# Kernel optimization log

Measured on AMD Instinct MI355X. Metric: run time of the kernel, lower is better.

The kernel has to match this reference:

```python
import jax, jax.numpy as jnp
import numpy as np

D_MODEL = 1024  # scaling uses sqrt(d_model), as in the source


def setup_inputs() -> dict:
    key = jax.random.key(0)
    kx, kq, kk, kv = jax.random.split(key, 4)
    B, N, D, H = 4, 4096, D_MODEL, 128
    X = jax.random.normal(kx, (B, N, D), dtype=jnp.float32)
    # nn.Linear(d_model, d_head, bias=False) weights, stored as [d_model, d_head]
    s = 1.0 / np.sqrt(D)
    Wq = jax.random.normal(kq, (D, H), dtype=jnp.float32) * s
    Wk = jax.random.normal(kk, (D, H), dtype=jnp.float32) * s
    Wv = jax.random.normal(kv, (D, H), dtype=jnp.float32) * s
    return {"X": X, "Wq": Wq, "Wk": Wk, "Wv": Wv}


def reference(X, Wq, Wk, Wv):
    # Q, K, V: [B, N, H]
    Q = jnp.einsum("bnd,dh->bnh", X, Wq)
    K = jnp.einsum("bnd,dh->bnh", X, Wk)
    V = jnp.einsum("bnd,dh->bnh", X, Wv)
    # Scores: [B, N, N]; source divides by sqrt(d_model) (not sqrt(d_head))
    A = jnp.einsum("bqh,bkh->bqk", Q, K) / jnp.sqrt(jnp.float32(D_MODEL))
    A = jax.nn.softmax(A, axis=-1)
    # Dropout is identity in eval mode (deterministic reference baseline)
    return jnp.einsum("bqk,bkh->bqh", A, V)
```

## Files before the change

### kernel.cpp

```cpp
#include <hip/hip_runtime.h>
#include <stdint.h>

typedef __bf16 bf16_t;
typedef bf16_t bf16x8 __attribute__((ext_vector_type(8)));
typedef float f32x4 __attribute__((ext_vector_type(4)));
typedef float f32x16 __attribute__((ext_vector_type(16)));
typedef unsigned short u16;
typedef unsigned int u32;

#define MFMA16(a, b, c) __builtin_amdgcn_mfma_f32_16x16x32_bf16((a), (b), (c), 0, 0, 0)
#define MFMA32(a, b, c) __builtin_amdgcn_mfma_f32_32x32x16_bf16((a), (b), (c), 0, 0, 0)

#define QSCALE 0.04508422002778633f

__device__ __forceinline__ u16 f2bf(float f) {
  union { float f; unsigned u; } v; v.f = f;
  unsigned r = v.u + 0x7fffu + ((v.u >> 16) & 1u);
  return (u16)(r >> 16);
}

__device__ __forceinline__ float exp2x(float x) {
#if __has_builtin(__builtin_amdgcn_exp2f)
  return __builtin_amdgcn_exp2f(x);
#else
  return exp2f(x);
#endif
}

__device__ __forceinline__ float rcpx(float x) {
#if __has_builtin(__builtin_amdgcn_rcpf)
  return __builtin_amdgcn_rcpf(x);
#else
  return 1.0f / x;
#endif
}

__device__ __forceinline__ void async_cp16(const void* g, void* l) {
  __builtin_amdgcn_global_load_lds(
      (__attribute__((address_space(1))) void*)(void*)g,
      (__attribute__((address_space(3))) void*)l, 16, 0, 0);
}

__device__ __forceinline__ u32 cvtpk(float lo, float hi) {
  u32 r;
  asm("v_cvt_pk_bf16_f32 %0, %1, %2" : "=v"(r) : "v"(lo), "v"(hi));
  return r;
}
__device__ __forceinline__ void pl32swap(u32& a, u32& b) {
  asm volatile("v_permlane32_swap_b32 %0, %1" : "+v"(a), "+v"(b));
}

__global__ __launch_bounds__(256) void pack_w_k(const float* __restrict__ Wq,
                                                const float* __restrict__ Wk,
                                                const float* __restrict__ Wv,
                                                u16* __restrict__ wp) {
  int t = blockIdx.x * 256 + threadIdx.x;
  int mat = t >> 14;
  int rr = t & 16383;
  int frag = rr >> 6, lane = rr & 63;
  int nt = frag >> 5, kc = frag & 31;
  const float* W = (mat == 0) ? Wq : ((mat == 1) ? Wk : Wv);
  int k0 = kc * 32 + ((lane >> 4) << 3);
  int col = nt * 16 + (lane & 15);
  union { u16 h[8]; uint4 q; } u_;
#pragma unroll
  for (int j = 0; j < 8; ++j) u_.h[j] = f2bf(W[(size_t)(k0 + j) * 128 + col]);
  *(uint4*)(wp + (size_t)t * 8) = u_.q;
}

__global__ __launch_bounds__(256) void qkv_k(const float* __restrict__ X,
                                             const u16* __restrict__ wp,
                                             u16* __restrict__ Qb,
                                             u16* __restrict__ Kb,
                                             u16* __restrict__ Vt) {
  __shared__ __align__(16) char xs[2][4096];
  const int tid = threadIdx.x;
  const int w = tid >> 6, lane = tid & 63;
  const int r16 = lane >> 4, c16 = lane & 15;
  const int m0 = blockIdx.x * 32;

  f32x4 acc[2][6];
#pragma unroll
  for (int mt = 0; mt < 2; ++mt)
#pragma unroll
    for (int i = 0; i < 6; ++i) acc[mt][i] = (f32x4){0.f, 0.f, 0.f, 0.f};

  const int srow = tid >> 3, scol = tid & 7;
  const float* sbase = X + (size_t)(m0 + srow) * 1024 + scol * 8;
  const int soff = srow * 128 + ((scol * 16) ^ ((srow & 7) << 4));

  {
    float4 v0 = *(const float4*)(sbase);
    float4 v1 = *(const float4*)(sbase + 4);
    union { u16 h[8]; uint4 q; } u_;
    u_.h[0] = f2bf(v0.x); u_.h[1] = f2bf(v0.y); u_.h[2] = f2bf(v0.z); u_.h[3] = f2bf(v0.w);
    u_.h[4] = f2bf(v1.x); u_.h[5] = f2bf(v1.y); u_.h[6] = f2bf(v1.z); u_.h[7] = f2bf(v1.w);
    *(uint4*)(xs[0] + soff) = u_.q;
  }
  __syncthreads();

  for (int kc = 0; kc < 16; ++kc) {
    float4 n0, n1;
    const bool pfch = (kc + 1) < 16;
    if (pfch) {
      n0 = *(const float4*)(sbase + (kc + 1) * 64);
      n1 = *(const float4*)(sbase + (kc + 1) * 64 + 4);
    }
    const char* xb = xs[kc & 1];
    bf16x8 a[2][2];
#pragma unroll
    for (int mt = 0; mt < 2; ++mt)
#pragma unroll
      for (int ks = 0; ks < 2; ++ks) {
        int row = mt * 16 + c16;
        int off = row * 128 + (((ks * 64) + r16 * 16) ^ ((row & 7) << 4));
        a[mt][ks] = *(const bf16x8*)(xb + off);
      }
#pragma unroll
    for (int i = 0; i < 6; ++i) {
      int t = w + 4 * i;
      int mat = t >> 3, nt = t & 7;
      const u16* bp = wp + (size_t)mat * 131072 +
                      (size_t)((nt * 32 + kc * 2) * 64 + lane) * 8;
#pragma unroll
      for (int ks = 0; ks < 2; ++ks) {
        bf16x8 b = *(const bf16x8*)(bp + (size_t)ks * 512);
#pragma unroll
        for (int mt = 0; mt < 2; ++mt) acc[mt][i] = MFMA16(a[mt][ks], b, acc[mt][i]);
      }
    }
    if (pfch) {
      union { u16 h[8]; uint4 q; } u_;
      u_.h[0] = f2bf(n0.x); u_.h[1] = f2bf(n0.y); u_.h[2] = f2bf(n0.z); u_.h[3] = f2bf(n0.w);
      u_.h[4] = f2bf(n1.x); u_.h[5] = f2bf(n1.y); u_.h[6] = f2bf(n1.z); u_.h[7] = f2bf(n1.w);
      *(uint4*)(xs[(kc + 1) & 1] + soff) = u_.q;
    }
    __syncthreads();
  }

  const int batch = m0 >> 12;
#pragma unroll
  for (int i = 0; i < 6; ++i) {
    int t = w + 4 * i;
    int mat = t >> 3, nt = t & 7;
#pragma unroll
    for (int mt = 0; mt < 2; ++mt) {
      f32x4 v = acc[mt][i];
      if (mat == 2) {
        int d = nt * 16 + c16;
        int nloc = (m0 & 4095) + mt * 16 + r16 * 4;
        union { u16 h[4]; uint2 q; } u_;
#pragma unroll
        for (int r = 0; r < 4; ++r) u_.h[r] = f2bf(v[r]);
        *(uint2*)(Vt + ((size_t)(batch * 128 + d)) * 4096 + nloc) = u_.q;
      } else {
        u16* dstm = (mat == 0) ? Qb : Kb;
        float sc = (mat == 0) ? QSCALE : 1.0f;
#pragma unroll
        for (int r = 0; r < 4; ++r) {
          int row = m0 + mt * 16 + r16 * 4 + r;
          dstm[(size_t)row * 128 + nt * 16 + c16] = f2bf(v[r] * sc);
        }
      }
    }
  }
}

__global__ __launch_bounds__(256) void pack_kv_k(const u16* __restrict__ Kb,
                                                 const u16* __restrict__ Vt,
                                                 u16* __restrict__ Kf,
                                                 u16* __restrict__ Vf) {
  int t = blockIdx.x * 256 + threadIdx.x;
  int lane = t & 63, l31 = lane & 31, hi = (lane >> 5) & 1;
  if (t < 262144) {
    int frag = t >> 6;
    int batch = frag >> 10, kt = (frag >> 3) & 127, kc = frag & 7;
    const u16* src = Kb + ((size_t)batch * 4096 + kt * 32 + l31) * 128 + kc * 16 + hi * 8;
    *(uint4*)(Kf + (size_t)t * 8) = *(const uint4*)src;
  } else {
    int o = t - 262144;
    int frag = o >> 6;
    int batch = frag >> 10, tt = (frag >> 4) & 63, ks = (frag >> 2) & 3, dt = frag & 3;
    const u16* src = Vt + ((size_t)batch * 128 + dt * 32 + l31) * 4096 + tt * 64 + ks * 16 + hi * 8;
    *(uint4*)(Vf + (size_t)o * 8) = *(const uint4*)src;
  }
}

__device__ __forceinline__ void stage16(const char* src, char* dst, int tid) {
#pragma unroll
  for (int i = 0; i < 4; ++i)
    async_cp16(src + i * 4096 + tid * 16, dst + i * 4096 + tid * 16);
}

__global__ __launch_bounds__(256, 3) void attn_k(const u16* __restrict__ Qb,
                                                 const u16* __restrict__ Kf,
                                                 const u16* __restrict__ Vf,
                                                 _Float16* __restrict__ Opart,
                                                 float* __restrict__ Ml,
                                                 int nsplit) {
  __shared__ __align__(16) char smem[49152];
  const int tid = threadIdx.x;
  const int w = tid >> 6, lane = tid & 63;
  const int l31 = lane & 31, hi = lane >> 5;

  const int B = gridDim.x;
  int xcd = blockIdx.x & 7, idx = blockIdx.x >> 3;
  int linear = xcd * (B >> 3) + idx;
  int qt = linear & 31, g = linear >> 5;
  int batch = g / nsplit, split = g - batch * nsplit;
  const int q0 = qt * 128;
  const int t0 = (split * 64) / nsplit;
  const int t1 = ((split + 1) * 64) / nsplit;
  const int T = t1 - t0;

  const char* kfc = (const char*)Kf + (size_t)batch * 1048576 + (size_t)t0 * 16384;
  const char* vfc = (const char*)Vf + (size_t)batch * 1048576 + (size_t)t0 * 16384;

  bf16x8 qf[8];
  const u16* qrow = Qb + ((size_t)batch * 4096 + q0 + w * 32 + l31) * 128 + hi * 8;
#pragma unroll
  for (int kc = 0; kc < 8; ++kc) qf[kc] = *(const bf16x8*)(qrow + kc * 16);

  f32x16 acc[4];
#pragma unroll
  for (int dt = 0; dt < 4; ++dt)
#pragma unroll
    for (int j = 0; j < 16; ++j) acc[dt][j] = 0.f;
  float lacc[8];
#pragma unroll
  for (int i = 0; i < 8; ++i) lacc[i] = 0.f;

  char* vbuf = smem + 32768;
  stage16(vfc, vbuf, tid);
  stage16(kfc, smem, tid);
  if (T > 1) stage16(kfc + 16384, smem + 16384, tid);

  for (int t = 0; t < T; ++t) {
    if (t + 1 < T) {
      asm volatile("s_waitcnt vmcnt(4)" ::: "memory");
    } else {
      asm volatile("s_waitcnt vmcnt(0)" ::: "memory");
    }
    __builtin_amdgcn_s_barrier();
    asm volatile("" ::: "memory");
    const char* kb = smem + (t & 1) * 16384;

    f32x16 sv[2];
    __builtin_amdgcn_s_setprio(1);
#pragma unroll
    for (int nt = 0; nt < 2; ++nt) {
      f32x16 s = {};
#pragma unroll
      for (int kc = 0; kc < 8; ++kc) {
        bf16x8 kf = *(const bf16x8*)(kb + (nt * 8 + kc) * 1024 + lane * 16);
        s = MFMA32(kf, qf[kc], s);
      }
      sv[nt] = s;
    }
    __builtin_amdgcn_s_setprio(0);

#pragma unroll
    for (int nt = 0; nt < 2; ++nt)
#pragma unroll
      for (int i = 0; i < 16; ++i) sv[nt][i] = exp2x(sv[nt][i]);
#pragma unroll
    for (int i = 0; i < 8; ++i)
      lacc[i] += (sv[0][i] + sv[0][i + 8]) + (sv[1][i] + sv[1][i + 8]);

    bf16x8 pf[4];
#pragma unroll
    for (int nt = 0; nt < 2; ++nt)
#pragma unroll
      for (int half = 0; half < 2; ++half) {
        const float* p = (const float*)&sv[nt] + half * 8;
        u32 a0 = cvtpk(p[0], p[1]);
        u32 b0 = cvtpk(p[4], p[5]);
        u32 c0 = cvtpk(p[2], p[3]);
        u32 d0 = cvtpk(p[6], p[7]);
        pl32swap(a0, b0);
        pl32swap(c0, d0);
        union { u32 u[4]; bf16x8 v; } pu;
        pu.u[0] = a0; pu.u[1] = c0; pu.u[2] = b0; pu.u[3] = d0;
        pf[nt * 2 + half] = pu.v;
      }

    __builtin_amdgcn_s_setprio(1);
#pragma unroll
    for (int dt = 0; dt < 4; ++dt) {
#pragma unroll
      for (int ks = 0; ks < 4; ++ks) {
        bf16x8 vf = *(const bf16x8*)(vbuf + (ks * 4 + dt) * 1024 + lane * 16);
        acc[dt] = MFMA32(pf[ks], vf, acc[dt]);
      }
    }
    __builtin_amdgcn_s_setprio(0);

    asm volatile("" ::: "memory");
    __builtin_amdgcn_s_barrier();
    asm volatile("" ::: "memory");

    if (t + 1 < T) stage16(vfc + (size_t)(t + 1) * 16384, vbuf, tid);
    if (t + 2 < T) stage16(kfc + (size_t)(t + 2) * 16384, smem + (t & 1) * 16384, tid);
  }

  float ltot = ((lacc[0] + lacc[1]) + (lacc[2] + lacc[3])) +
               ((lacc[4] + lacc[5]) + (lacc[6] + lacc[7]));
  ltot += __shfl_xor(ltot, 32);

  size_t obase = (size_t)split * 16384 + (size_t)batch * 4096 + q0 + w * 32;
#pragma unroll
  for (int dt = 0; dt < 4; ++dt)
#pragma unroll
    for (int r = 0; r < 16; ++r) {
      int qr = (r & 3) + 8 * (r >> 2) + 4 * hi;
      float lq = __shfl(ltot, qr);
      Opart[(obase + qr) * 128 + dt * 32 + l31] = (_Float16)(acc[dt][r] * rcpx(lq));
    }
  if (lane < 32)
    Ml[(size_t)split * 16384 + (size_t)batch * 4096 + q0 + w * 32 + lane] = ltot;
}

template <int S>
__global__ __launch_bounds__(256) void reduce_k(const _Float16* __restrict__ Op,
                                                const float* __restrict__ Ml,
                                                float* __restrict__ Out) {
  int t = blockIdx.x * 256 + threadIdx.x;
  int q = t >> 4, d8 = (t & 15) << 3;
  float ls[S];
  float L = 0.f;
#pragma unroll
  for (int s = 0; s < S; ++s) {
    ls[s] = Ml[(size_t)s * 16384 + q];
    L += ls[s];
  }
  float o[8] = {0.f, 0.f, 0.f, 0.f, 0.f, 0.f, 0.f, 0.f};
#pragma unroll
  for (int s = 0; s < S; ++s) {
    union { uint4 u; _Float16 h[8]; } pv;
    pv.u = *(const uint4*)(Op + ((size_t)s * 16384 + q) * 128 + d8);
#pragma unroll
    for (int j = 0; j < 8; ++j) o[j] += (float)pv.h[j] * ls[s];
  }
  float inv = rcpx(L);
  float4 r0 = {o[0] * inv, o[1] * inv, o[2] * inv, o[3] * inv};
  float4 r1 = {o[4] * inv, o[5] * inv, o[6] * inv, o[7] * inv};
  *(float4*)(Out + (size_t)q * 128 + d8) = r0;
  *(float4*)(Out + (size_t)q * 128 + d8 + 4) = r1;
}

extern "C" void kernel_launch(void* const* d_in, const int* in_sizes, int n_in,
                              void* d_out, int out_size, void* d_ws, size_t ws_size,
                              hipStream_t stream) {
  const float* X  = (const float*)d_in[0];
  const float* Wq = (const float*)d_in[1];
  const float* Wk = (const float*)d_in[2];
  const float* Wv = (const float*)d_in[3];
  float* Out = (float*)d_out;
  char* ws = (char*)d_ws;
  u16* Qb = (u16*)(ws);
  u16* Kf = (u16*)(ws + (4u << 20));
  u16* Vf = (u16*)(ws + (8u << 20));
  _Float16* Opart = (_Float16*)(ws + (12u << 20));
  u16* Kb = (u16*)(ws + (12u << 20));
  u16* Vt = (u16*)(ws + (16u << 20));
  u16* Wp = (u16*)(ws + (20u << 20));

  int S = (ws_size >= (12ull << 20) + 6ull * (4194304ull + 65536ull)) ? 6 : 4;
  float* Ml = (float*)(ws + (12ull << 20) + (size_t)S * 4194304ull);

  pack_w_k<<<dim3(192), dim3(256), 0, stream>>>(Wq, Wk, Wv, Wp);
  qkv_k<<<dim3(512), dim3(256), 0, stream>>>(X, Wp, Qb, Kb, Vt);
  pack_kv_k<<<dim3(2048), dim3(256), 0, stream>>>(Kb, Vt, Kf, Vf);
  attn_k<<<dim3(128 * S), dim3(256), 0, stream>>>(Qb, Kf, Vf, Opart, Ml, S);
  if (S == 6)
    reduce_k<6><<<dim3(1024), dim3(256), 0, stream>>>(Opart, Ml, Out);
  else
    reduce_k<4><<<dim3(1024), dim3(256), 0, stream>>>(Opart, Ml, Out);
}
```

Baseline: 96.34 us.

## Double attention query tile per block, async-stage fp32 X in projection

The attention kernel now processes 256 query rows per block, with each wave handling two 32-row query sub-tiles. This halves the K/V tile loads per query and doubles MFMA work per staged K/V tile. To keep the grid size reasonable, the split count rises to 8 and occupancy drops to 2 blocks per CU. The QKV projection now async-copies raw fp32 X into swizzled shared memory, converts to bf16 at fragment load, and hoists the weight fragment loads ahead of the MFMAs. Costs: higher register pressure, lower occupancy, larger partial-output workspace, and a waitcnt on all copies each iteration.

```diff
diff --git a/kernel.cpp b/kernel.cpp
--- a/kernel.cpp
+++ b/kernel.cpp
@@ -68,16 +68,29 @@
   *(uint4*)(wp + (size_t)t * 8) = u_.q;
 }
 
+__device__ __forceinline__ void qkv_stage(const char* Xb, char* dst, int m0,
+                                          int kc, int tid) {
+#pragma unroll
+  for (int i = 0; i < 2; ++i) {
+    int p = i * 4096 + tid * 16;
+    int row = p >> 8, cb = p & 255;
+    int ucb = cb ^ ((row & 7) << 4);
+    async_cp16(Xb + ((size_t)(m0 + row) * 4096 + (size_t)kc * 256 + ucb),
+               dst + p);
+  }
+}
+
 __global__ __launch_bounds__(256) void qkv_k(const float* __restrict__ X,
                                              const u16* __restrict__ wp,
                                              u16* __restrict__ Qb,
                                              u16* __restrict__ Kb,
                                              u16* __restrict__ Vt) {
-  __shared__ __align__(16) char xs[2][4096];
+  __shared__ __align__(16) char xs[2][8192];
   const int tid = threadIdx.x;
   const int w = tid >> 6, lane = tid & 63;
   const int r16 = lane >> 4, c16 = lane & 15;
   const int m0 = blockIdx.x * 32;
+  const char* Xb = (const char*)X;
 
   f32x4 acc[2][6];
 #pragma unroll
@@ -85,57 +98,49 @@
 #pragma unroll
     for (int i = 0; i < 6; ++i) acc[mt][i] = (f32x4){0.f, 0.f, 0.f, 0.f};
 
-  const int srow = tid >> 3, scol = tid & 7;
-  const float* sbase = X + (size_t)(m0 + srow) * 1024 + scol * 8;
-  const int soff = srow * 128 + ((scol * 16) ^ ((srow & 7) << 4));
-
-  {
-    float4 v0 = *(const float4*)(sbase);
-    float4 v1 = *(const float4*)(sbase + 4);
-    union { u16 h[8]; uint4 q; } u_;
-    u_.h[0] = f2bf(v0.x); u_.h[1] = f2bf(v0.y); u_.h[2] = f2bf(v0.z); u_.h[3] = f2bf(v0.w);
-    u_.h[4] = f2bf(v1.x); u_.h[5] = f2bf(v1.y); u_.h[6] = f2bf(v1.z); u_.h[7] = f2bf(v1.w);
-    *(uint4*)(xs[0] + soff) = u_.q;
-  }
-  __syncthreads();
+  qkv_stage(Xb, xs[0], m0, 0, tid);
 
   for (int kc = 0; kc < 16; ++kc) {
-    float4 n0, n1;
-    const bool pfch = (kc + 1) < 16;
-    if (pfch) {
-      n0 = *(const float4*)(sbase + (kc + 1) * 64);
-      n1 = *(const float4*)(sbase + (kc + 1) * 64 + 4);
-    }
+    asm volatile("s_waitcnt vmcnt(0)" ::: "memory");
+    __builtin_amdgcn_s_barrier();
+    asm volatile("" ::: "memory");
+    if (kc + 1 < 16) qkv_stage(Xb, xs[(kc + 1) & 1], m0, kc + 1, tid);
+
     const char* xb = xs[kc & 1];
-    bf16x8 a[2][2];
-#pragma unroll
-    for (int mt = 0; mt < 2; ++mt)
-#pragma unroll
-      for (int ks = 0; ks < 2; ++ks) {
-        int row = mt * 16 + c16;
-        int off = row * 128 + (((ks * 64) + r16 * 16) ^ ((row & 7) << 4));
-        a[mt][ks] = *(const bf16x8*)(xb + off);
-      }
+    bf16x8 bw[6][2];
 #pragma unroll
     for (int i = 0; i < 6; ++i) {
       int t = w + 4 * i;
       int mat = t >> 3, nt = t & 7;
       const u16* bp = wp + (size_t)mat * 131072 +
                       (size_t)((nt * 32 + kc * 2) * 64 + lane) * 8;
+      bw[i][0] = *(const bf16x8*)(bp);
+      bw[i][1] = *(const bf16x8*)(bp + 512);
+    }
+    bf16x8 a[2][2];
+#pragma unroll
+    for (int mt = 0; mt < 2; ++mt)
 #pragma unroll
       for (int ks = 0; ks < 2; ++ks) {
-        bf16x8 b = *(const bf16x8*)(bp + (size_t)ks * 512);
-#pragma unroll
-        for (int mt = 0; mt < 2; ++mt) acc[mt][i] = MFMA16(a[mt][ks], b, acc[mt][i]);
-      }
-    }
-    if (pfch) {
-      union { u16 h[8]; uint4 q; } u_;
-      u_.h[0] = f2bf(n0.x); u_.h[1] = f2bf(n0.y); u_.h[2] = f2bf(n0.z); u_.h[3] = f2bf(n0.w);
-      u_.h[4] = f2bf(n1.x); u_.h[5] = f2bf(n1.y); u_.h[6] = f2bf(n1.z); u_.h[7] = f2bf(n1.w);
-      *(uint4*)(xs[(kc + 1) & 1] + soff) = u_.q;
-    }
-    __syncthreads();
+        int row = mt * 16 + c16;
+        int swz = (row & 7) << 4;
+        int cb0 = ks * 128 + r16 * 32;
+        f32x4 lo = *(const f32x4*)(xb + row * 256 + (cb0 ^ swz));
+        f32x4 hi = *(const f32x4*)(xb + row * 256 + ((cb0 + 16) ^ swz));
+        union { u32 u[4]; bf16x8 v; } pu;
+        pu.u[0] = cvtpk(lo[0], lo[1]);
+        pu.u[1] = cvtpk(lo[2], lo[3]);
+        pu.u[2] = cvtpk(hi[0], hi[1]);
+        pu.u[3] = cvtpk(hi[2], hi[3]);
+        a[mt][ks] = pu.v;
+      }
+#pragma unroll
+    for (int i = 0; i < 6; ++i)
+#pragma unroll
+      for (int ks = 0; ks < 2; ++ks)
+#pragma unroll
+        for (int mt = 0; mt < 2; ++mt)
+          acc[mt][i] = MFMA16(a[mt][ks], bw[i][ks], acc[mt][i]);
   }
 
   const int batch = m0 >> 12;
@@ -192,7 +197,7 @@
     async_cp16(src + i * 4096 + tid * 16, dst + i * 4096 + tid * 16);
 }
 
-__global__ __launch_bounds__(256, 3) void attn_k(const u16* __restrict__ Qb,
+__global__ __launch_bounds__(256, 2) void attn_k(const u16* __restrict__ Qb,
                                                  const u16* __restrict__ Kf,
                                                  const u16* __restrict__ Vf,
                                                  _Float16* __restrict__ Opart,
@@ -206,29 +211,32 @@
   const int B = gridDim.x;
   int xcd = blockIdx.x & 7, idx = blockIdx.x >> 3;
   int linear = xcd * (B >> 3) + idx;
-  int qt = linear & 31, g = linear >> 5;
+  int qt = linear & 15, g = linear >> 4;
   int batch = g / nsplit, split = g - batch * nsplit;
-  const int q0 = qt * 128;
-  const int t0 = (split * 64) / nsplit;
-  const int t1 = ((split + 1) * 64) / nsplit;
-  const int T = t1 - t0;
+  const int q0 = qt * 256;
+  const int T = 64 / nsplit;
+  const int t0 = split * T;
 
   const char* kfc = (const char*)Kf + (size_t)batch * 1048576 + (size_t)t0 * 16384;
   const char* vfc = (const char*)Vf + (size_t)batch * 1048576 + (size_t)t0 * 16384;
 
-  bf16x8 qf[8];
-  const u16* qrow = Qb + ((size_t)batch * 4096 + q0 + w * 32 + l31) * 128 + hi * 8;
-#pragma unroll
-  for (int kc = 0; kc < 8; ++kc) qf[kc] = *(const bf16x8*)(qrow + kc * 16);
-
-  f32x16 acc[4];
+  bf16x8 qf0[8], qf1[8];
+  const u16* qrow0 = Qb + ((size_t)batch * 4096 + q0 + w * 64 + l31) * 128 + hi * 8;
+  const u16* qrow1 = qrow0 + 32 * 128;
+#pragma unroll
+  for (int kc = 0; kc < 8; ++kc) {
+    qf0[kc] = *(const bf16x8*)(qrow0 + kc * 16);
+    qf1[kc] = *(const bf16x8*)(qrow1 + kc * 16);
+  }
+
+  f32x16 accA[4], accB[4];
 #pragma unroll
   for (int dt = 0; dt < 4; ++dt)
 #pragma unroll
-    for (int j = 0; j < 16; ++j) acc[dt][j] = 0.f;
-  float lacc[8];
-#pragma unroll
-  for (int i = 0; i < 8; ++i) lacc[i] = 0.f;
+    for (int j = 0; j < 16; ++j) { accA[dt][j] = 0.f; accB[dt][j] = 0.f; }
+  float lacc0[4], lacc1[4];
+#pragma unroll
+  for (int i = 0; i < 4; ++i) { lacc0[i] = 0.f; lacc1[i] = 0.f; }
 
   char* vbuf = smem + 32768;
   stage16(vfc, vbuf, tid);
@@ -245,44 +253,83 @@
     asm volatile("" ::: "memory");
     const char* kb = smem + (t & 1) * 16384;
 
-    f32x16 sv[2];
-    __builtin_amdgcn_s_setprio(1);
-#pragma unroll
-    for (int nt = 0; nt < 2; ++nt) {
-      f32x16 s = {};
+    bf16x8 pf0[4], pf1[4];
+    {
+      f32x16 svA = {}, svB = {};
+      __builtin_amdgcn_s_setprio(1);
 #pragma unroll
       for (int kc = 0; kc < 8; ++kc) {
-        bf16x8 kf = *(const bf16x8*)(kb + (nt * 8 + kc) * 1024 + lane * 16);
-        s = MFMA32(kf, qf[kc], s);
-      }
-      sv[nt] = s;
-    }
-    __builtin_amdgcn_s_setprio(0);
-
-#pragma unroll
-    for (int nt = 0; nt < 2; ++nt)
-#pragma unroll
-      for (int i = 0; i < 16; ++i) sv[nt][i] = exp2x(sv[nt][i]);
-#pragma unroll
-    for (int i = 0; i < 8; ++i)
-      lacc[i] += (sv[0][i] + sv[0][i + 8]) + (sv[1][i] + sv[1][i + 8]);
-
-    bf16x8 pf[4];
-#pragma unroll
-    for (int nt = 0; nt < 2; ++nt)
+        bf16x8 kf = *(const bf16x8*)(kb + kc * 1024 + lane * 16);
+        svA = MFMA32(kf, qf0[kc], svA);
+      }
+#pragma unroll
+      for (int kc = 0; kc < 8; ++kc) {
+        bf16x8 kf = *(const bf16x8*)(kb + (8 + kc) * 1024 + lane * 16);
+        svB = MFMA32(kf, qf0[kc], svB);
+      }
+      __builtin_amdgcn_s_setprio(0);
+#pragma unroll
+      for (int i = 0; i < 16; ++i) { svA[i] = exp2x(svA[i]); svB[i] = exp2x(svB[i]); }
+#pragma unroll
+      for (int i = 0; i < 4; ++i)
+        lacc0[i] += ((svA[i] + svA[i + 4]) + (svA[i + 8] + svA[i + 12])) +
+                    ((svB[i] + svB[i + 4]) + (svB[i + 8] + svB[i + 12]));
 #pragma unroll
       for (int half = 0; half < 2; ++half) {
-        const float* p = (const float*)&sv[nt] + half * 8;
-        u32 a0 = cvtpk(p[0], p[1]);
-        u32 b0 = cvtpk(p[4], p[5]);
-        u32 c0 = cvtpk(p[2], p[3]);
-        u32 d0 = cvtpk(p[6], p[7]);
-        pl32swap(a0, b0);
-        pl32swap(c0, d0);
+        const float* pA = (const float*)&svA + half * 8;
+        const float* pB = (const float*)&svB + half * 8;
+        u32 a0 = cvtpk(pA[0], pA[1]), b0 = cvtpk(pA[4], pA[5]);
+        u32 c0 = cvtpk(pA[2], pA[3]), d0 = cvtpk(pA[6], pA[7]);
+        pl32swap(a0, b0); pl32swap(c0, d0);
         union { u32 u[4]; bf16x8 v; } pu;
         pu.u[0] = a0; pu.u[1] = c0; pu.u[2] = b0; pu.u[3] = d0;
-        pf[nt * 2 + half] = pu.v;
-      }
+        pf0[half] = pu.v;
+        u32 a1 = cvtpk(pB[0], pB[1]), b1 = cvtpk(pB[4], pB[5]);
+        u32 c1 = cvtpk(pB[2], pB[3]), d1 = cvtpk(pB[6], pB[7]);
+        pl32swap(a1, b1); pl32swap(c1, d1);
+        union { u32 u[4]; bf16x8 v; } pv;
+        pv.u[0] = a1; pv.u[1] = c1; pv.u[2] = b1; pv.u[3] = d1;
+        pf0[2 + half] = pv.v;
+      }
+    }
+    {
+      f32x16 svA = {}, svB = {};
+      __builtin_amdgcn_s_setprio(1);
+#pragma unroll
+      for (int kc = 0; kc < 8; ++kc) {
+        bf16x8 kf = *(const bf16x8*)(kb + kc * 1024 + lane * 16);
+        svA = MFMA32(kf, qf1[kc], svA);
+      }
+#pragma unroll
+      for (int kc = 0; kc < 8; ++kc) {
+        bf16x8 kf = *(const bf16x8*)(kb + (8 + kc) * 1024 + lane * 16);
+        svB = MFMA32(kf, qf1[kc], svB);
+      }
+      __builtin_amdgcn_s_setprio(0);
+#pragma unroll
+      for (int i = 0; i < 16; ++i) { svA[i] = exp2x(svA[i]); svB[i] = exp2x(svB[i]); }
+#pragma unroll
+      for (int i = 0; i < 4; ++i)
+        lacc1[i] += ((svA[i] + svA[i + 4]) + (svA[i + 8] + svA[i + 12])) +
+                    ((svB[i] + svB[i + 4]) + (svB[i + 8] + svB[i + 12]));
+#pragma unroll
+      for (int half = 0; half < 2; ++half) {
+        const float* pA = (const float*)&svA + half * 8;
+        const float* pB = (const float*)&svB + half * 8;
+        u32 a0 = cvtpk(pA[0], pA[1]), b0 = cvtpk(pA[4], pA[5]);
+        u32 c0 = cvtpk(pA[2], pA[3]), d0 = cvtpk(pA[6], pA[7]);
+        pl32swap(a0, b0); pl32swap(c0, d0);
+        union { u32 u[4]; bf16x8 v; } pu;
+        pu.u[0] = a0; pu.u[1] = c0; pu.u[2] = b0; pu.u[3] = d0;
+        pf1[half] = pu.v;
+        u32 a1 = cvtpk(pB[0], pB[1]), b1 = cvtpk(pB[4], pB[5]);
+        u32 c1 = cvtpk(pB[2], pB[3]), d1 = cvtpk(pB[6], pB[7]);
+        pl32swap(a1, b1); pl32swap(c1, d1);
+        union { u32 u[4]; bf16x8 v; } pv;
+        pv.u[0] = a1; pv.u[1] = c1; pv.u[2] = b1; pv.u[3] = d1;
+        pf1[2 + half] = pv.v;
+      }
+    }
 
     __builtin_amdgcn_s_setprio(1);
 #pragma unroll
@@ -290,7 +337,8 @@
 #pragma unroll
       for (int ks = 0; ks < 4; ++ks) {
         bf16x8 vf = *(const bf16x8*)(vbuf + (ks * 4 + dt) * 1024 + lane * 16);
-        acc[dt] = MFMA32(pf[ks], vf, acc[dt]);
+        accA[dt] = MFMA32(pf0[ks], vf, accA[dt]);
+        accB[dt] = MFMA32(pf1[ks], vf, accB[dt]);
       }
     }
     __builtin_amdgcn_s_setprio(0);
@@ -303,21 +351,27 @@
     if (t + 2 < T) stage16(kfc + (size_t)(t + 2) * 16384, smem + (t & 1) * 16384, tid);
   }
 
-  float ltot = ((lacc[0] + lacc[1]) + (lacc[2] + lacc[3])) +
-               ((lacc[4] + lacc[5]) + (lacc[6] + lacc[7]));
-  ltot += __shfl_xor(ltot, 32);
-
-  size_t obase = (size_t)split * 16384 + (size_t)batch * 4096 + q0 + w * 32;
+  float lt0 = (lacc0[0] + lacc0[1]) + (lacc0[2] + lacc0[3]);
+  float lt1 = (lacc1[0] + lacc1[1]) + (lacc1[2] + lacc1[3]);
+  lt0 += __shfl_xor(lt0, 32);
+  lt1 += __shfl_xor(lt1, 32);
+
+  size_t ob = (size_t)split * 16384 + (size_t)batch * 4096 + q0 + w * 64;
 #pragma unroll
   for (int dt = 0; dt < 4; ++dt)
 #pragma unroll
     for (int r = 0; r < 16; ++r) {
       int qr = (r & 3) + 8 * (r >> 2) + 4 * hi;
-      float lq = __shfl(ltot, qr);
-      Opart[(obase + qr) * 128 + dt * 32 + l31] = (_Float16)(acc[dt][r] * rcpx(lq));
-    }
-  if (lane < 32)
-    Ml[(size_t)split * 16384 + (size_t)batch * 4096 + q0 + w * 32 + lane] = ltot;
+      float lq0 = __shfl(lt0, qr);
+      Opart[(ob + qr) * 128 + dt * 32 + l31] = (_Float16)(accA[dt][r] * rcpx(lq0));
+      float lq1 = __shfl(lt1, qr);
+      Opart[(ob + 32 + qr) * 128 + dt * 32 + l31] = (_Float16)(accB[dt][r] * rcpx(lq1));
+    }
+  if (lane < 32) {
+    size_t mb = (size_t)split * 16384 + (size_t)batch * 4096 + q0 + w * 64 + lane;
+    Ml[mb] = lt0;
+    Ml[mb + 32] = lt1;
+  }
 }
 
 template <int S>
@@ -365,15 +419,15 @@
   u16* Vt = (u16*)(ws + (16u << 20));
   u16* Wp = (u16*)(ws + (20u << 20));
 
-  int S = (ws_size >= (12ull << 20) + 6ull * (4194304ull + 65536ull)) ? 6 : 4;
+  int S = (ws_size >= (12ull << 20) + 8ull * (4194304ull + 65536ull)) ? 8 : 4;
   float* Ml = (float*)(ws + (12ull << 20) + (size_t)S * 4194304ull);
 
   pack_w_k<<<dim3(192), dim3(256), 0, stream>>>(Wq, Wk, Wv, Wp);
   qkv_k<<<dim3(512), dim3(256), 0, stream>>>(X, Wp, Qb, Kb, Vt);
   pack_kv_k<<<dim3(2048), dim3(256), 0, stream>>>(Kb, Vt, Kf, Vf);
-  attn_k<<<dim3(128 * S), dim3(256), 0, stream>>>(Qb, Kf, Vf, Opart, Ml, S);
-  if (S == 6)
-    reduce_k<6><<<dim3(1024), dim3(256), 0, stream>>>(Opart, Ml, Out);
+  attn_k<<<dim3(64 * S), dim3(256), 0, stream>>>(Qb, Kf, Vf, Opart, Ml, S);
+  if (S == 8)
+    reduce_k<8><<<dim3(1024), dim3(256), 0, stream>>>(Opart, Ml, Out);
   else
     reduce_k<4><<<dim3(1024), dim3(256), 0, stream>>>(Opart, Ml, Out);
 }
```

After: 143.4 us. +48.8%, slower.
